# Kernel optimization log

Hardware: AMD Instinct MI355X
Metric: run time of the kernel (lower is better)

The kernel has to match this reference:

```python
import jax, jax.numpy as jnp
import numpy as np

N_HEAD = 16
N_KV_HEAD = 4


def setup_inputs() -> dict:
    key = jax.random.key(0)
    ks = jax.random.split(key, 5)
    B, T, D = 2, 2048, 2048
    kdim = D // N_HEAD  # 128
    s = 0.02
    x = jax.random.normal(ks[0], (B, T, D), dtype=jnp.float32)
    Wq = jax.random.normal(ks[1], (D, D), dtype=jnp.float32) * s
    Wk = jax.random.normal(ks[2], (D, N_KV_HEAD * kdim), dtype=jnp.float32) * s
    Wv = jax.random.normal(ks[3], (D, N_KV_HEAD * kdim), dtype=jnp.float32) * s
    Wo = jax.random.normal(ks[4], (D, D), dtype=jnp.float32) * s
    return {"x": x, "Wq": Wq, "Wk": Wk, "Wv": Wv, "Wo": Wo}


def reference(x, Wq, Wk, Wv, Wo):
    B, T, D = x.shape
    h, kv = N_HEAD, N_KV_HEAD
    g = h // kv  # query groups per kv head
    kdim = D // h
    Q = (x @ Wq).reshape(B, T, h, kdim).transpose(0, 2, 1, 3)   # [B,h,T,k]
    K = (x @ Wk).reshape(B, T, kv, kdim).transpose(0, 2, 1, 3)  # [B,kv,T,k]
    V = (x @ Wv).reshape(B, T, kv, kdim).transpose(0, 2, 1, 3)
    # repeat_interleave(g, dim=1): kv outer, group inner
    K = jnp.broadcast_to(K[:, :, None], (B, kv, g, T, kdim)).reshape(B, h, T, kdim)
    V = jnp.broadcast_to(V[:, :, None], (B, kv, g, T, kdim)).reshape(B, h, T, kdim)
    scores = jnp.einsum('bhqd,bhkd->bhqk', Q, K) / jnp.sqrt(jnp.float32(kdim))
    causal = jnp.tril(jnp.ones((T, T), dtype=bool))
    scores = jnp.where(causal[None, None], scores, jnp.float32(-jnp.inf))
    A = jax.nn.softmax(scores, axis=-1)
    Y = jnp.einsum('bhqk,bhkd->bhqd', A, V).transpose(0, 2, 1, 3).reshape(B, T, D)
    return Y @ Wo
```

## Files before the change

### kernel.cpp

```cpp
#include <hip/hip_runtime.h>
#include <hip/hip_bf16.h>

typedef __bf16 bf16x8 __attribute__((ext_vector_type(8)));
typedef float f32x4 __attribute__((ext_vector_type(4)));

__device__ __forceinline__ unsigned short f2bf(float f) {
  unsigned int u = __float_as_uint(f);
  u += 0x7fffu + ((u >> 16) & 1u);
  return (unsigned short)(u >> 16);
}

__device__ __forceinline__ unsigned int pack2(float lo, float hi) {
  __hip_bfloat162 h = __float22bfloat162_rn(float2{lo, hi});
  return *(unsigned int*)&h;
}

__device__ __forceinline__ void load_lds16(const void* g, void* l) {
  __builtin_amdgcn_global_load_lds(
      (const __attribute__((address_space(1))) unsigned int*)g,
      (__attribute__((address_space(3))) unsigned int*)l, 16, 0, 0);
}

__global__ void cvt_x(const float* __restrict__ in, unsigned short* __restrict__ out) {
  size_t i = ((size_t)blockIdx.x * 256 + threadIdx.x) * 4;
  float4 v = *(const float4*)(in + i);
  ushort4 o;
  o.x = f2bf(v.x); o.y = f2bf(v.y); o.z = f2bf(v.z); o.w = f2bf(v.w);
  *(ushort4*)(out + i) = o;
}

__global__ void tr_w(const float* __restrict__ in, unsigned short* __restrict__ out,
                     int ldin, int ldout) {
  __shared__ float tile[32][33];
  const int c0 = blockIdx.x * 32, r0 = blockIdx.y * 32;
  const int tx = threadIdx.x, ty = threadIdx.y;
#pragma unroll
  for (int j = 0; j < 4; ++j)
    tile[ty + j * 8][tx] = in[(size_t)(r0 + ty + j * 8) * ldin + c0 + tx];
  __syncthreads();
#pragma unroll
  for (int j = 0; j < 4; ++j)
    out[(size_t)(c0 + ty + j * 8) * ldout + r0 + tx] = f2bf(tile[tx][ty + j * 8]);
}

__global__ void tr_v(const unsigned short* __restrict__ QKV, unsigned short* __restrict__ VT) {
  __shared__ unsigned short tile[32][33];
  const int z = blockIdx.z, b = z >> 2, kvh = z & 3;
  const unsigned short* in = QKV + (size_t)(b * 2048) * 3072 + 2560 + kvh * 128;
  unsigned short* out = VT + (size_t)z * 128 * 2048;
  const int c0 = blockIdx.x * 32, r0 = blockIdx.y * 32;
  const int tx = threadIdx.x, ty = threadIdx.y;
#pragma unroll
  for (int j = 0; j < 4; ++j)
    tile[ty + j * 8][tx] = in[(size_t)(r0 + ty + j * 8) * 3072 + c0 + tx];
  __syncthreads();
#pragma unroll
  for (int j = 0; j < 4; ++j)
    out[(size_t)(c0 + ty + j * 8) * 2048 + r0 + tx] = tile[tx][ty + j * 8];
}

template <int NF, int OUTF32>
__global__ __launch_bounds__(512, 2) void gemm256(const unsigned short* __restrict__ A,
                                                  const unsigned short* __restrict__ B,
                                                  void* __restrict__ Cv, int M, int N, int K) {
  __shared__ __attribute__((aligned(16))) unsigned short Ah[2][2][256 * 32];
  __shared__ __attribute__((aligned(16))) unsigned short Bf[2][64 * NF * 64];
  const int tid = threadIdx.x;
  const int lane = tid & 63;
  const int cl = lane & 15, rg = lane >> 4;
  const int wave = tid >> 6;
  const int wm = wave >> 2, wn = wave & 3;
  const int bm = blockIdx.y, bn = blockIdx.x;
  const int NK = K >> 6;
  const int rowA = bm * 256, rowB = bn * (64 * NF);

  f32x4 acc[8][NF] = {};

  auto stage_A = [&](int bf, int h, int kt) {
#pragma unroll
    for (int i = 0; i < 2; ++i) {
      const int L = i * 512 + tid;
      const int r = L >> 2;
      const int c = (L & 3) ^ ((r >> 1) & 3);
      load_lds16(A + (size_t)(rowA + r) * K + kt * 64 + h * 32 + c * 8,
                 &Ah[bf][h][(size_t)(i * 512 + (tid & ~63)) * 8]);
    }
  };
  auto stage_B = [&](int bf, int kt) {
#pragma unroll
    for (int i = 0; i < NF; ++i) {
      const int L = i * 512 + tid;
      const int r = L >> 3;
      const int c = (L & 7) ^ (r & 7);
      load_lds16(B + (size_t)(rowB + r) * K + kt * 64 + c * 8,
                 &Bf[bf][(size_t)(i * 512 + (tid & ~63)) * 8]);
    }
  };

  stage_B(0, 0);
  stage_A(0, 0, 0);
  stage_A(0, 1, 0);
  __syncthreads();

  int buf = 0;
#pragma unroll 1
  for (int kt = 0; kt < NK; ++kt) {
    const bool nl = (kt + 1 < NK);
    if (nl) {
      stage_B(buf ^ 1, kt + 1);
      stage_A(buf ^ 1, 0, kt + 1);
      stage_A(buf ^ 1, 1, kt + 1);
    }
    {
      bf16x8 af[8], bfr[NF];
#pragma unroll
      for (int f = 0; f < 8; ++f) {
        const int r = 128 * wm + 16 * f + cl;
        af[f] = *(const bf16x8*)(&Ah[buf][0][(r * 4 + (rg ^ ((r >> 1) & 3))) * 8]);
      }
#pragma unroll
      for (int nf = 0; nf < NF; ++nf) {
        const int r = 16 * NF * wn + 16 * nf + cl;
        bfr[nf] = *(const bf16x8*)(&Bf[buf][(r * 8 + (rg ^ (r & 7))) * 8]);
      }
      __builtin_amdgcn_s_setprio(1);
#pragma unroll
      for (int f = 0; f < 8; ++f)
#pragma unroll
        for (int nf = 0; nf < NF; ++nf)
          acc[f][nf] = __builtin_amdgcn_mfma_f32_16x16x32_bf16(af[f], bfr[nf], acc[f][nf], 0, 0, 0);
      __builtin_amdgcn_s_setprio(0);
    }
    {
      bf16x8 af[8], bfr[NF];
#pragma unroll
      for (int f = 0; f < 8; ++f) {
        const int r = 128 * wm + 16 * f + cl;
        af[f] = *(const bf16x8*)(&Ah[buf][1][(r * 4 + (rg ^ ((r >> 1) & 3))) * 8]);
      }
#pragma unroll
      for (int nf = 0; nf < NF; ++nf) {
        const int r = 16 * NF * wn + 16 * nf + cl;
        bfr[nf] = *(const bf16x8*)(&Bf[buf][(r * 8 + ((4 + rg) ^ (r & 7))) * 8]);
      }
      __builtin_amdgcn_s_setprio(1);
#pragma unroll
      for (int f = 0; f < 8; ++f)
#pragma unroll
        for (int nf = 0; nf < NF; ++nf)
          acc[f][nf] = __builtin_amdgcn_mfma_f32_16x16x32_bf16(af[f], bfr[nf], acc[f][nf], 0, 0, 0);
      __builtin_amdgcn_s_setprio(0);
    }
    __syncthreads();
    buf ^= 1;
  }

#pragma unroll
  for (int f = 0; f < 8; ++f)
#pragma unroll
    for (int nf = 0; nf < NF; ++nf)
#pragma unroll
      for (int i = 0; i < 4; ++i) {
        const int row = bm * 256 + wm * 128 + f * 16 + rg * 4 + i;
        const int col = bn * 64 * NF + wn * 16 * NF + nf * 16 + cl;
        if (OUTF32)
          ((float*)Cv)[(size_t)row * N + col] = acc[f][nf][i];
        else
          ((unsigned short*)Cv)[(size_t)row * N + col] = f2bf(acc[f][nf][i]);
      }
}

__global__ __launch_bounds__(256, 2) void attn(const unsigned short* __restrict__ QKV,
                                               const unsigned short* __restrict__ VT,
                                               unsigned short* __restrict__ O) {
  __shared__ __attribute__((aligned(16))) unsigned short Ks[2][64 * 128];
  __shared__ __attribute__((aligned(16))) unsigned short VTs[2][128 * 64];
  const int T = 2048, LD = 3072, D = 2048;
  const int jp = blockIdx.x, h = blockIdx.y, b = blockIdx.z;
  const int kvh = h >> 2;
  const int tid = threadIdx.x, lane = tid & 63, wave = tid >> 6;
  const int cl = lane & 15, rg = lane >> 4;
  const bool abit = (lane & 16) != 0, bbit = (lane & 32) != 0;
  const bool ab = abit != bbit;
  const unsigned short* Kbase = QKV + (size_t)b * T * LD + 2048 + kvh * 128;
  const unsigned short* Vbase = VT + (size_t)(b * 4 + kvh) * 128 * T;

  auto stage = [&](int sb, int k0) {
#pragma unroll
    for (int i = 0; i < 4; ++i) {
      const int Ls = i * 256 + tid;
      const int r = Ls >> 4, s = Ls & 15, c = s ^ (r & 7);
      load_lds16(Kbase + (size_t)(k0 + r) * LD + c * 8,
                 &Ks[sb][(i * 256 + (tid & 0xC0)) * 8]);
    }
#pragma unroll
    for (int i = 0; i < 4; ++i) {
      const int Ls = i * 256 + tid;
      const int r = Ls >> 3, s = Ls & 7, c = s ^ (r & 7);
      load_lds16(Vbase + (size_t)r * T + k0 + c * 8,
                 &VTs[sb][(i * 256 + (tid & 0xC0)) * 8]);
    }
  };

  const float scale = 0.08838834764831845f;

#pragma unroll 1
  for (int pass = 0; pass < 2; ++pass) {
    const int jt = pass ? (31 - jp) : jp;
    const int q0 = jt * 64;
    const int nkt = jt + 1;
    const int qrow = q0 + wave * 16 + cl;

    const unsigned short* Qp = QKV + (size_t)(b * T + qrow) * LD + h * 128;
    bf16x8 qf[4];
#pragma unroll
    for (int ks = 0; ks < 4; ++ks) qf[ks] = *(const bf16x8*)(Qp + ks * 32 + rg * 8);

    f32x4 o[8] = {};
    float m = -1e30f, l = 0.f;
    int buf = 0;

    stage(0, 0);
    __syncthreads();

#pragma unroll 1
    for (int kt = 0; kt < nkt; ++kt) {
      if (kt + 1 < nkt) stage(buf ^ 1, (kt + 1) * 64);

      f32x4 sa[4] = {};
      __builtin_amdgcn_s_setprio(1);
#pragma unroll
      for (int ks = 0; ks < 4; ++ks) {
#pragma unroll
        for (int n = 0; n < 4; ++n) {
          const int row = n * 16 + cl;
          const int p = (ks * 4 + rg) ^ (row & 7);
          const bf16x8 kf = *(const bf16x8*)(&Ks[buf][row * 128 + p * 8]);
          sa[n] = __builtin_amdgcn_mfma_f32_16x16x32_bf16(kf, qf[ks], sa[n], 0, 0, 0);
        }
      }
      __builtin_amdgcn_s_setprio(0);

      const int k0 = kt * 64;
      float p[4][4];
      float pmax = -1e30f;
      if (kt == jt) {
#pragma unroll
        for (int n = 0; n < 4; ++n)
#pragma unroll
          for (int i = 0; i < 4; ++i) {
            const int kg = k0 + n * 16 + rg * 4 + i;
            p[n][i] = (kg > qrow) ? -1e30f : sa[n][i] * scale;
            pmax = fmaxf(pmax, p[n][i]);
          }
      } else {
#pragma unroll
        for (int n = 0; n < 4; ++n)
#pragma unroll
          for (int i = 0; i < 4; ++i) {
            p[n][i] = sa[n][i] * scale;
            pmax = fmaxf(pmax, p[n][i]);
          }
      }
      pmax = fmaxf(pmax, __shfl_xor(pmax, 16));
      pmax = fmaxf(pmax, __shfl_xor(pmax, 32));

      if (!__all(pmax <= m + 8.f)) {
        const float mnew = fmaxf(m, pmax);
        const float alpha = __expf(m - mnew);
        m = mnew;
        l *= alpha;
#pragma unroll
        for (int n2 = 0; n2 < 8; ++n2) o[n2] *= alpha;
      }

      float rs = 0.f;
#pragma unroll
      for (int n = 0; n < 4; ++n)
#pragma unroll
        for (int i = 0; i < 4; ++i) {
          p[n][i] = __expf(p[n][i] - m);
          rs += p[n][i];
        }
      rs += __shfl_xor(rs, 16);
      rs += __shfl_xor(rs, 32);
      l += rs;

      unsigned int F[2][4];
#pragma unroll
      for (int ks2 = 0; ks2 < 2; ++ks2) {
        const unsigned int pk00 = pack2(p[2 * ks2][0], p[2 * ks2][1]);
        const unsigned int pk01 = pack2(p[2 * ks2][2], p[2 * ks2][3]);
        const unsigned int pk10 = pack2(p[2 * ks2 + 1][0], p[2 * ks2 + 1][1]);
        const unsigned int pk11 = pack2(p[2 * ks2 + 1][2], p[2 * ks2 + 1][3]);
        const unsigned int s0 = bbit ? pk00 : pk10;
        const unsigned int s1 = bbit ? pk01 : pk11;
        const unsigned int r0 = (unsigned int)__shfl_xor((int)s0, 32);
        const unsigned int r1 = (unsigned int)__shfl_xor((int)s1, 32);
        const unsigned int gk0 = bbit ? pk10 : pk00;
        const unsigned int gk1 = bbit ? pk11 : pk01;
        const unsigned int t0 = ab ? gk0 : r0;
        const unsigned int t1 = ab ? gk1 : r1;
        const unsigned int u0 = (unsigned int)__shfl_xor((int)t0, 16);
        const unsigned int u1 = (unsigned int)__shfl_xor((int)t1, 16);
        const unsigned int k20 = ab ? r0 : gk0;
        const unsigned int k21 = ab ? r1 : gk1;
        F[ks2][0] = abit ? u0 : k20;
        F[ks2][1] = abit ? u1 : k21;
        F[ks2][2] = abit ? k20 : u0;
        F[ks2][3] = abit ? k21 : u1;
      }

      __builtin_amdgcn_s_setprio(1);
#pragma unroll
      for (int ks2 = 0; ks2 < 2; ++ks2) {
        uint4 fu = make_uint4(F[ks2][0], F[ks2][1], F[ks2][2], F[ks2][3]);
        const bf16x8 pf = *(const bf16x8*)&fu;
#pragma unroll
        for (int n2 = 0; n2 < 8; ++n2) {
          const int dr = n2 * 16 + cl;
          const int p2 = (ks2 * 4 + rg) ^ (dr & 7);
          const bf16x8 vf = *(const bf16x8*)(&VTs[buf][dr * 64 + p2 * 8]);
          o[n2] = __builtin_amdgcn_mfma_f32_16x16x32_bf16(vf, pf, o[n2], 0, 0, 0);
        }
      }
      __builtin_amdgcn_s_setprio(0);

      __syncthreads();
      buf ^= 1;
    }

    const float rl = __builtin_amdgcn_rcpf(l);
#pragma unroll
    for (int n2 = 0; n2 < 8; ++n2) {
      ushort4 ov;
      ov.x = f2bf(o[n2][0] * rl);
      ov.y = f2bf(o[n2][1] * rl);
      ov.z = f2bf(o[n2][2] * rl);
      ov.w = f2bf(o[n2][3] * rl);
      *(ushort4*)(O + (size_t)(b * T + qrow) * D + h * 128 + n2 * 16 + rg * 4) = ov;
    }
  }
}

extern "C" void kernel_launch(void* const* d_in, const int* in_sizes, int n_in,
                              void* d_out, int out_size, void* d_ws, size_t ws_size,
                              hipStream_t stream) {
  const float* x = (const float*)d_in[0];
  const float* Wq = (const float*)d_in[1];
  const float* Wk = (const float*)d_in[2];
  const float* Wv = (const float*)d_in[3];
  const float* Wo = (const float*)d_in[4];
  float* out = (float*)d_out;

  char* ws = (char*)d_ws;
  unsigned short* xb    = (unsigned short*)(ws);
  unsigned short* WqkvT = (unsigned short*)(ws + 16777216);
  unsigned short* WoT   = (unsigned short*)(ws + 29360128);
  unsigned short* QKV   = (unsigned short*)(ws + 37748736);
  unsigned short* VTb   = (unsigned short*)(ws + 62914560);

  cvt_x<<<dim3(8192), dim3(256), 0, stream>>>(x, xb);
  tr_w<<<dim3(64, 64), dim3(32, 8), 0, stream>>>(Wq, WqkvT, 2048, 2048);
  tr_w<<<dim3(16, 64), dim3(32, 8), 0, stream>>>(Wk, WqkvT + (size_t)2048 * 2048, 512, 2048);
  tr_w<<<dim3(16, 64), dim3(32, 8), 0, stream>>>(Wv, WqkvT + (size_t)2560 * 2048, 512, 2048);
  tr_w<<<dim3(64, 64), dim3(32, 8), 0, stream>>>(Wo, WoT, 2048, 2048);

  gemm256<3, 0><<<dim3(16, 16), dim3(512), 0, stream>>>(xb, WqkvT, QKV, 4096, 3072, 2048);
  tr_v<<<dim3(4, 64, 8), dim3(32, 8), 0, stream>>>(QKV, VTb);
  attn<<<dim3(16, 16, 2), dim3(256), 0, stream>>>(QKV, VTb, xb);
  gemm256<2, 1><<<dim3(16, 16), dim3(512), 0, stream>>>(xb, WoT, out, 4096, 2048, 2048);
}
```

Measured before the change: 200.4 us.

## Add 256x256-tile 8-phase ping-pong GEMM for the QKV projection

Adds a new GEMM kernel with 256x256 output tiles whose K loop is split into eight phases. Each phase interleaves LDS fragment reads and global-to-LDS prefetches with MFMA quarter-blocks, using explicit barriers and waitcnt fences. The QKV projection now uses it with a 12x16 grid instead of the 192-wide tile kernel on a 16x16 grid, raising arithmetic intensity per block and overlapping memory with compute. In exchange there are fewer blocks (192) on a GPU with many CUs, the manual waitcnt scheduling is fragile, and register pressure rises. Alongside this, unsigned short is renamed to a short alias.

```diff
diff --git a/kernel.cpp b/kernel.cpp
--- a/kernel.cpp
+++ b/kernel.cpp
@@ -3,11 +3,12 @@
 
 typedef __bf16 bf16x8 __attribute__((ext_vector_type(8)));
 typedef float f32x4 __attribute__((ext_vector_type(4)));
-
-__device__ __forceinline__ unsigned short f2bf(float f) {
+typedef unsigned short us;
+
+__device__ __forceinline__ us f2bf(float f) {
   unsigned int u = __float_as_uint(f);
   u += 0x7fffu + ((u >> 16) & 1u);
-  return (unsigned short)(u >> 16);
+  return (us)(u >> 16);
 }
 
 __device__ __forceinline__ unsigned int pack2(float lo, float hi) {
@@ -21,7 +22,7 @@
       (__attribute__((address_space(3))) unsigned int*)l, 16, 0, 0);
 }
 
-__global__ void cvt_x(const float* __restrict__ in, unsigned short* __restrict__ out) {
+__global__ void cvt_x(const float* __restrict__ in, us* __restrict__ out) {
   size_t i = ((size_t)blockIdx.x * 256 + threadIdx.x) * 4;
   float4 v = *(const float4*)(in + i);
   ushort4 o;
@@ -29,7 +30,7 @@
   *(ushort4*)(out + i) = o;
 }
 
-__global__ void tr_w(const float* __restrict__ in, unsigned short* __restrict__ out,
+__global__ void tr_w(const float* __restrict__ in, us* __restrict__ out,
                      int ldin, int ldout) {
   __shared__ float tile[32][33];
   const int c0 = blockIdx.x * 32, r0 = blockIdx.y * 32;
@@ -43,11 +44,11 @@
     out[(size_t)(c0 + ty + j * 8) * ldout + r0 + tx] = f2bf(tile[tx][ty + j * 8]);
 }
 
-__global__ void tr_v(const unsigned short* __restrict__ QKV, unsigned short* __restrict__ VT) {
-  __shared__ unsigned short tile[32][33];
+__global__ void tr_v(const us* __restrict__ QKV, us* __restrict__ VT) {
+  __shared__ us tile[32][33];
   const int z = blockIdx.z, b = z >> 2, kvh = z & 3;
-  const unsigned short* in = QKV + (size_t)(b * 2048) * 3072 + 2560 + kvh * 128;
-  unsigned short* out = VT + (size_t)z * 128 * 2048;
+  const us* in = QKV + (size_t)(b * 2048) * 3072 + 2560 + kvh * 128;
+  us* out = VT + (size_t)z * 128 * 2048;
   const int c0 = blockIdx.x * 32, r0 = blockIdx.y * 32;
   const int tx = threadIdx.x, ty = threadIdx.y;
 #pragma unroll
@@ -59,12 +60,153 @@
     out[(size_t)(c0 + ty + j * 8) * 2048 + r0 + tx] = tile[tx][ty + j * 8];
 }
 
+template <int OUTF32>
+__global__ __launch_bounds__(512, 2) void gemm8p(const us* __restrict__ A,
+                                                 const us* __restrict__ B,
+                                                 void* __restrict__ Cv,
+                                                 int M, int N, int K) {
+  __shared__ __attribute__((aligned(16))) us As[2][2][128 * 64];
+  __shared__ __attribute__((aligned(16))) us Bs[2][2][128 * 64];
+  const int tid = threadIdx.x;
+  const int lane = tid & 63;
+  const int cl = lane & 15, rg = lane >> 4;
+  const int wave = tid >> 6;
+  const int wm = wave >> 2, wn = wave & 3;
+  const int bm = blockIdx.y, bn = blockIdx.x;
+  const int NK = K >> 6;
+  const int rowA = bm * 256, rowB = bn * 256;
+
+  f32x4 acc[8][4] = {};
+
+  auto stA = [&](int bf, int h, int kt) {
+#pragma unroll
+    for (int i = 0; i < 2; ++i) {
+      const int L = i * 512 + tid;
+      const int r = L >> 3, c = (L & 7) ^ (r & 7);
+      load_lds16(A + (size_t)(rowA + h * 128 + r) * K + kt * 64 + c * 8,
+                 &As[bf][h][(i * 512 + (tid & ~63)) * 8]);
+    }
+  };
+  auto stB = [&](int bf, int h, int kt) {
+#pragma unroll
+    for (int i = 0; i < 2; ++i) {
+      const int L = i * 512 + tid;
+      const int r = L >> 3, c = (L & 7) ^ (r & 7);
+      load_lds16(B + (size_t)(rowB + h * 128 + r) * K + kt * 64 + c * 8,
+                 &Bs[bf][h][(i * 512 + (tid & ~63)) * 8]);
+    }
+  };
+
+  const int pxor = cl & 7;
+  bf16x8 aA[4][2], bA[2][2], bB[2][2];
+
+  auto rdA = [&](int bf, int fq) {
+#pragma unroll
+    for (int f = 0; f < 4; ++f) {
+      const int r = fq * 64 + f * 16 + cl;
+#pragma unroll
+      for (int ks = 0; ks < 2; ++ks)
+        aA[f][ks] = *(const bf16x8*)(&As[bf][wm][(r * 8 + ((ks * 4 + rg) ^ pxor)) * 8]);
+    }
+  };
+  auto rdB = [&](bf16x8 (&b)[2][2], int bf, int nq) {
+#pragma unroll
+    for (int j = 0; j < 2; ++j) {
+      const int r = (wn & 1) * 64 + (nq * 2 + j) * 16 + cl;
+#pragma unroll
+      for (int ks = 0; ks < 2; ++ks)
+        b[j][ks] = *(const bf16x8*)(&Bs[bf][wn >> 1][(r * 8 + ((ks * 4 + rg) ^ pxor)) * 8]);
+    }
+  };
+  auto mmQ = [&](bf16x8 (&b)[2][2], int fq, int nq) {
+    __builtin_amdgcn_s_setprio(1);
+#pragma unroll
+    for (int f = 0; f < 4; ++f)
+#pragma unroll
+      for (int j = 0; j < 2; ++j)
+#pragma unroll
+        for (int ks = 0; ks < 2; ++ks)
+          acc[fq * 4 + f][nq * 2 + j] = __builtin_amdgcn_mfma_f32_16x16x32_bf16(
+              aA[f][ks], b[j][ks], acc[fq * 4 + f][nq * 2 + j], 0, 0, 0);
+    __builtin_amdgcn_s_setprio(0);
+  };
+
+#define BAR __builtin_amdgcn_s_barrier()
+#define LGK0 asm volatile("s_waitcnt lgkmcnt(0)" ::: "memory")
+#define VM4 asm volatile("s_waitcnt vmcnt(4)" ::: "memory")
+#define VM0 asm volatile("s_waitcnt vmcnt(0)" ::: "memory")
+
+  stA(0, 0, 0); stB(0, 0, 0); stA(0, 1, 0); stB(0, 1, 0);
+  stB(1, 0, 1); stA(1, 0, 1);
+  VM4;
+  BAR;
+
+#pragma unroll 1
+  for (int T = 0; T < NK; T += 2) {
+    const bool s34 = (T + 2) < NK, s78 = (T + 3) < NK;
+
+    rdA(0, 0); rdB(bA, 0, 0);
+    stA(1, 1, T + 1);
+    asm volatile("s_waitcnt lgkmcnt(8)" ::: "memory");
+    BAR; LGK0; mmQ(bA, 0, 0); BAR;
+
+    rdB(bB, 0, 1);
+    stB(1, 1, T + 1);
+    BAR; LGK0; mmQ(bB, 0, 1); BAR;
+
+    rdA(0, 1);
+    if (s34) stB(0, 0, T + 2);
+    BAR; LGK0; mmQ(bA, 1, 0); BAR;
+
+    if (s34) stA(0, 0, T + 2);
+    BAR; mmQ(bB, 1, 1);
+    if (s34) { VM4; } else { VM0; }
+    BAR;
+
+    rdA(1, 0); rdB(bA, 1, 0);
+    if (s34) stB(0, 1, T + 2);
+    asm volatile("s_waitcnt lgkmcnt(8)" ::: "memory");
+    BAR; LGK0; mmQ(bA, 0, 0); BAR;
+
+    rdB(bB, 1, 1);
+    if (s34) stA(0, 1, T + 2);
+    BAR; LGK0; mmQ(bB, 0, 1); BAR;
+
+    rdA(1, 1);
+    if (s78) stB(1, 0, T + 3);
+    BAR; LGK0; mmQ(bA, 1, 0); BAR;
+
+    if (s78) stA(1, 0, T + 3);
+    BAR; mmQ(bB, 1, 1);
+    if (s78) { VM4; } else { VM0; }
+    BAR;
+  }
+#undef BAR
+#undef LGK0
+#undef VM4
+#undef VM0
+
+#pragma unroll
+  for (int f = 0; f < 8; ++f)
+#pragma unroll
+    for (int nf = 0; nf < 4; ++nf)
+#pragma unroll
+      for (int i = 0; i < 4; ++i) {
+        const int row = bm * 256 + wm * 128 + f * 16 + rg * 4 + i;
+        const int col = bn * 256 + wn * 64 + nf * 16 + cl;
+        if (OUTF32)
+          ((float*)Cv)[(size_t)row * N + col] = acc[f][nf][i];
+        else
+          ((us*)Cv)[(size_t)row * N + col] = f2bf(acc[f][nf][i]);
+      }
+}
+
 template <int NF, int OUTF32>
-__global__ __launch_bounds__(512, 2) void gemm256(const unsigned short* __restrict__ A,
-                                                  const unsigned short* __restrict__ B,
+__global__ __launch_bounds__(512, 2) void gemm256(const us* __restrict__ A,
+                                                  const us* __restrict__ B,
                                                   void* __restrict__ Cv, int M, int N, int K) {
-  __shared__ __attribute__((aligned(16))) unsigned short Ah[2][2][256 * 32];
-  __shared__ __attribute__((aligned(16))) unsigned short Bf[2][64 * NF * 64];
+  __shared__ __attribute__((aligned(16))) us Ah[2][2][256 * 32];
+  __shared__ __attribute__((aligned(16))) us Bf[2][64 * NF * 64];
   const int tid = threadIdx.x;
   const int lane = tid & 63;
   const int cl = lane & 15, rg = lane >> 4;
@@ -166,15 +308,15 @@
         if (OUTF32)
           ((float*)Cv)[(size_t)row * N + col] = acc[f][nf][i];
         else
-          ((unsigned short*)Cv)[(size_t)row * N + col] = f2bf(acc[f][nf][i]);
-      }
-}
-
-__global__ __launch_bounds__(256, 2) void attn(const unsigned short* __restrict__ QKV,
-                                               const unsigned short* __restrict__ VT,
-                                               unsigned short* __restrict__ O) {
-  __shared__ __attribute__((aligned(16))) unsigned short Ks[2][64 * 128];
-  __shared__ __attribute__((aligned(16))) unsigned short VTs[2][128 * 64];
+          ((us*)Cv)[(size_t)row * N + col] = f2bf(acc[f][nf][i]);
+      }
+}
+
+__global__ __launch_bounds__(256, 2) void attn(const us* __restrict__ QKV,
+                                               const us* __restrict__ VT,
+                                               us* __restrict__ O) {
+  __shared__ __attribute__((aligned(16))) us Ks[2][64 * 128];
+  __shared__ __attribute__((aligned(16))) us VTs[2][128 * 64];
   const int T = 2048, LD = 3072, D = 2048;
   const int jp = blockIdx.x, h = blockIdx.y, b = blockIdx.z;
   const int kvh = h >> 2;
@@ -182,8 +324,8 @@
   const int cl = lane & 15, rg = lane >> 4;
   const bool abit = (lane & 16) != 0, bbit = (lane & 32) != 0;
   const bool ab = abit != bbit;
-  const unsigned short* Kbase = QKV + (size_t)b * T * LD + 2048 + kvh * 128;
-  const unsigned short* Vbase = VT + (size_t)(b * 4 + kvh) * 128 * T;
+  const us* Kbase = QKV + (size_t)b * T * LD + 2048 + kvh * 128;
+  const us* Vbase = VT + (size_t)(b * 4 + kvh) * 128 * T;
 
   auto stage = [&](int sb, int k0) {
 #pragma unroll
@@ -211,7 +353,7 @@
     const int nkt = jt + 1;
     const int qrow = q0 + wave * 16 + cl;
 
-    const unsigned short* Qp = QKV + (size_t)(b * T + qrow) * LD + h * 128;
+    const us* Qp = QKV + (size_t)(b * T + qrow) * LD + h * 128;
     bf16x8 qf[4];
 #pragma unroll
     for (int ks = 0; ks < 4; ++ks) qf[ks] = *(const bf16x8*)(Qp + ks * 32 + rg * 8);
@@ -354,11 +496,11 @@
   float* out = (float*)d_out;
 
   char* ws = (char*)d_ws;
-  unsigned short* xb    = (unsigned short*)(ws);
-  unsigned short* WqkvT = (unsigned short*)(ws + 16777216);
-  unsigned short* WoT   = (unsigned short*)(ws + 29360128);
-  unsigned short* QKV   = (unsigned short*)(ws + 37748736);
-  unsigned short* VTb   = (unsigned short*)(ws + 62914560);
+  us* xb    = (us*)(ws);
+  us* WqkvT = (us*)(ws + 16777216);
+  us* WoT   = (us*)(ws + 29360128);
+  us* QKV   = (us*)(ws + 37748736);
+  us* VTb   = (us*)(ws + 62914560);
 
   cvt_x<<<dim3(8192), dim3(256), 0, stream>>>(x, xb);
   tr_w<<<dim3(64, 64), dim3(32, 8), 0, stream>>>(Wq, WqkvT, 2048, 2048);
@@ -366,7 +508,7 @@
   tr_w<<<dim3(16, 64), dim3(32, 8), 0, stream>>>(Wv, WqkvT + (size_t)2560 * 2048, 512, 2048);
   tr_w<<<dim3(64, 64), dim3(32, 8), 0, stream>>>(Wo, WoT, 2048, 2048);
 
-  gemm256<3, 0><<<dim3(16, 16), dim3(512), 0, stream>>>(xb, WqkvT, QKV, 4096, 3072, 2048);
+  gemm8p<0><<<dim3(12, 16), dim3(512), 0, stream>>>(xb, WqkvT, QKV, 4096, 3072, 2048);
   tr_v<<<dim3(4, 64, 8), dim3(32, 8), 0, stream>>>(QKV, VTb);
   attn<<<dim3(16, 16, 2), dim3(256), 0, stream>>>(QKV, VTb, xb);
   gemm256<2, 1><<<dim3(16, 16), dim3(512), 0, stream>>>(xb, WoT, out, 4096, 2048, 2048);
```

Result: slower. 208.4 us (+4.0%).

## Split causal attention key range into two halves with 128-row query tiles and merge

Applied to the files above, without the earlier changes.

Each attention block now handles a 128-row query tile, with each wave processing two 16-row subtiles. Every K/V fragment read from LDS therefore feeds two MFMAs. The causal key range of each tile is split into two equal halves run by separate blocks, which balances work per block. The halves write unnormalized bf16 partial outputs plus running max/sum, and a new merge_o kernel rescales and combines them. This costs an extra kernel launch and extra global traffic for the partials, which are stored in the output buffer and the freed weight workspace.

```diff
diff --git a/kernel.cpp b/kernel.cpp
--- a/kernel.cpp
+++ b/kernel.cpp
@@ -3,11 +3,16 @@
 
 typedef __bf16 bf16x8 __attribute__((ext_vector_type(8)));
 typedef float f32x4 __attribute__((ext_vector_type(4)));
-
-__device__ __forceinline__ unsigned short f2bf(float f) {
+typedef unsigned short us;
+
+__device__ __forceinline__ us f2bf(float f) {
   unsigned int u = __float_as_uint(f);
   u += 0x7fffu + ((u >> 16) & 1u);
-  return (unsigned short)(u >> 16);
+  return (us)(u >> 16);
+}
+
+__device__ __forceinline__ float bf2f(us u) {
+  return __uint_as_float(((unsigned int)u) << 16);
 }
 
 __device__ __forceinline__ unsigned int pack2(float lo, float hi) {
@@ -21,7 +26,7 @@
       (__attribute__((address_space(3))) unsigned int*)l, 16, 0, 0);
 }
 
-__global__ void cvt_x(const float* __restrict__ in, unsigned short* __restrict__ out) {
+__global__ void cvt_x(const float* __restrict__ in, us* __restrict__ out) {
   size_t i = ((size_t)blockIdx.x * 256 + threadIdx.x) * 4;
   float4 v = *(const float4*)(in + i);
   ushort4 o;
@@ -29,7 +34,7 @@
   *(ushort4*)(out + i) = o;
 }
 
-__global__ void tr_w(const float* __restrict__ in, unsigned short* __restrict__ out,
+__global__ void tr_w(const float* __restrict__ in, us* __restrict__ out,
                      int ldin, int ldout) {
   __shared__ float tile[32][33];
   const int c0 = blockIdx.x * 32, r0 = blockIdx.y * 32;
@@ -43,11 +48,11 @@
     out[(size_t)(c0 + ty + j * 8) * ldout + r0 + tx] = f2bf(tile[tx][ty + j * 8]);
 }
 
-__global__ void tr_v(const unsigned short* __restrict__ QKV, unsigned short* __restrict__ VT) {
-  __shared__ unsigned short tile[32][33];
+__global__ void tr_v(const us* __restrict__ QKV, us* __restrict__ VT) {
+  __shared__ us tile[32][33];
   const int z = blockIdx.z, b = z >> 2, kvh = z & 3;
-  const unsigned short* in = QKV + (size_t)(b * 2048) * 3072 + 2560 + kvh * 128;
-  unsigned short* out = VT + (size_t)z * 128 * 2048;
+  const us* in = QKV + (size_t)(b * 2048) * 3072 + 2560 + kvh * 128;
+  us* out = VT + (size_t)z * 128 * 2048;
   const int c0 = blockIdx.x * 32, r0 = blockIdx.y * 32;
   const int tx = threadIdx.x, ty = threadIdx.y;
 #pragma unroll
@@ -60,11 +65,11 @@
 }
 
 template <int NF, int OUTF32>
-__global__ __launch_bounds__(512, 2) void gemm256(const unsigned short* __restrict__ A,
-                                                  const unsigned short* __restrict__ B,
+__global__ __launch_bounds__(512, 2) void gemm256(const us* __restrict__ A,
+                                                  const us* __restrict__ B,
                                                   void* __restrict__ Cv, int M, int N, int K) {
-  __shared__ __attribute__((aligned(16))) unsigned short Ah[2][2][256 * 32];
-  __shared__ __attribute__((aligned(16))) unsigned short Bf[2][64 * NF * 64];
+  __shared__ __attribute__((aligned(16))) us Ah[2][2][256 * 32];
+  __shared__ __attribute__((aligned(16))) us Bf[2][64 * NF * 64];
   const int tid = threadIdx.x;
   const int lane = tid & 63;
   const int cl = lane & 15, rg = lane >> 4;
@@ -166,26 +171,30 @@
         if (OUTF32)
           ((float*)Cv)[(size_t)row * N + col] = acc[f][nf][i];
         else
-          ((unsigned short*)Cv)[(size_t)row * N + col] = f2bf(acc[f][nf][i]);
-      }
-}
-
-__global__ __launch_bounds__(256, 2) void attn(const unsigned short* __restrict__ QKV,
-                                               const unsigned short* __restrict__ VT,
-                                               unsigned short* __restrict__ O) {
-  __shared__ __attribute__((aligned(16))) unsigned short Ks[2][64 * 128];
-  __shared__ __attribute__((aligned(16))) unsigned short VTs[2][128 * 64];
-  const int T = 2048, LD = 3072, D = 2048;
-  const int jp = blockIdx.x, h = blockIdx.y, b = blockIdx.z;
+          ((us*)Cv)[(size_t)row * N + col] = f2bf(acc[f][nf][i]);
+      }
+}
+
+__global__ __launch_bounds__(256, 2) void attn(const us* __restrict__ QKV,
+                                               const us* __restrict__ VT,
+                                               us* __restrict__ Opart,
+                                               float2* __restrict__ ML) {
+  __shared__ __attribute__((aligned(16))) us Ks[2][64 * 128];
+  __shared__ __attribute__((aligned(16))) us VTs[2][128 * 64];
+  const int T = 2048, LD = 3072;
+  const int jt = 15 - (blockIdx.x & 15);
+  const int half = blockIdx.x >> 4;
+  const int h = blockIdx.y, b = blockIdx.z;
   const int kvh = h >> 2;
   const int tid = threadIdx.x, lane = tid & 63, wave = tid >> 6;
   const int cl = lane & 15, rg = lane >> 4;
   const bool abit = (lane & 16) != 0, bbit = (lane & 32) != 0;
   const bool ab = abit != bbit;
-  const unsigned short* Kbase = QKV + (size_t)b * T * LD + 2048 + kvh * 128;
-  const unsigned short* Vbase = VT + (size_t)(b * 4 + kvh) * 128 * T;
-
-  auto stage = [&](int sb, int k0) {
+  const us* Kbase = QKV + (size_t)b * T * LD + 2048 + kvh * 128;
+  const us* Vbase = VT + (size_t)(b * 4 + kvh) * 128 * T;
+
+  auto stage = [&](int sb, int kt) {
+    const int k0 = kt * 64;
 #pragma unroll
     for (int i = 0; i < 4; ++i) {
       const int Ls = i * 256 + tid;
@@ -203,75 +212,82 @@
   };
 
   const float scale = 0.08838834764831845f;
+  const int q0 = jt * 128;
+  const int qb = q0 + wave * 32;
+  const int kb = half ? (jt + 1) : 0;
+  const int ke = half ? (2 * jt + 2) : (jt + 1);
+
+  bf16x8 qf[2][4];
+#pragma unroll
+  for (int sub = 0; sub < 2; ++sub) {
+    const us* Qp = QKV + (size_t)(b * T + qb + sub * 16 + cl) * LD + h * 128;
+#pragma unroll
+    for (int ks = 0; ks < 4; ++ks) qf[sub][ks] = *(const bf16x8*)(Qp + ks * 32 + rg * 8);
+  }
+
+  f32x4 o[2][8] = {};
+  float mrun[2] = {-1e30f, -1e30f}, lrun[2] = {0.f, 0.f};
+  int buf = 0;
+
+  stage(0, kb);
+  __syncthreads();
 
 #pragma unroll 1
-  for (int pass = 0; pass < 2; ++pass) {
-    const int jt = pass ? (31 - jp) : jp;
-    const int q0 = jt * 64;
-    const int nkt = jt + 1;
-    const int qrow = q0 + wave * 16 + cl;
-
-    const unsigned short* Qp = QKV + (size_t)(b * T + qrow) * LD + h * 128;
-    bf16x8 qf[4];
-#pragma unroll
-    for (int ks = 0; ks < 4; ++ks) qf[ks] = *(const bf16x8*)(Qp + ks * 32 + rg * 8);
-
-    f32x4 o[8] = {};
-    float m = -1e30f, l = 0.f;
-    int buf = 0;
-
-    stage(0, 0);
-    __syncthreads();
-
-#pragma unroll 1
-    for (int kt = 0; kt < nkt; ++kt) {
-      if (kt + 1 < nkt) stage(buf ^ 1, (kt + 1) * 64);
-
-      f32x4 sa[4] = {};
-      __builtin_amdgcn_s_setprio(1);
-#pragma unroll
-      for (int ks = 0; ks < 4; ++ks) {
-#pragma unroll
-        for (int n = 0; n < 4; ++n) {
-          const int row = n * 16 + cl;
-          const int p = (ks * 4 + rg) ^ (row & 7);
-          const bf16x8 kf = *(const bf16x8*)(&Ks[buf][row * 128 + p * 8]);
-          sa[n] = __builtin_amdgcn_mfma_f32_16x16x32_bf16(kf, qf[ks], sa[n], 0, 0, 0);
-        }
-      }
-      __builtin_amdgcn_s_setprio(0);
-
-      const int k0 = kt * 64;
-      float p[4][4];
+  for (int kt = kb; kt < ke; ++kt) {
+    if (kt + 1 < ke) stage(buf ^ 1, kt + 1);
+
+    f32x4 sa[2][4] = {};
+    __builtin_amdgcn_s_setprio(1);
+#pragma unroll
+    for (int ks = 0; ks < 4; ++ks) {
+#pragma unroll
+      for (int n = 0; n < 4; ++n) {
+        const int row = n * 16 + cl;
+        const int p = (ks * 4 + rg) ^ (row & 7);
+        const bf16x8 kf = *(const bf16x8*)(&Ks[buf][row * 128 + p * 8]);
+        sa[0][n] = __builtin_amdgcn_mfma_f32_16x16x32_bf16(kf, qf[0][ks], sa[0][n], 0, 0, 0);
+        sa[1][n] = __builtin_amdgcn_mfma_f32_16x16x32_bf16(kf, qf[1][ks], sa[1][n], 0, 0, 0);
+      }
+    }
+    __builtin_amdgcn_s_setprio(0);
+
+    const int k0 = kt * 64;
+    float p[2][4][4];
+    unsigned int F[2][2][4];
+
+#pragma unroll
+    for (int sub = 0; sub < 2; ++sub) {
+      const int qbs = qb + sub * 16;
+      const int qrow = qbs + cl;
       float pmax = -1e30f;
-      if (kt == jt) {
+      if (k0 + 63 > qbs) {
 #pragma unroll
         for (int n = 0; n < 4; ++n)
 #pragma unroll
           for (int i = 0; i < 4; ++i) {
             const int kg = k0 + n * 16 + rg * 4 + i;
-            p[n][i] = (kg > qrow) ? -1e30f : sa[n][i] * scale;
-            pmax = fmaxf(pmax, p[n][i]);
+            p[sub][n][i] = (kg > qrow) ? -1e30f : sa[sub][n][i] * scale;
+            pmax = fmaxf(pmax, p[sub][n][i]);
           }
       } else {
 #pragma unroll
         for (int n = 0; n < 4; ++n)
 #pragma unroll
           for (int i = 0; i < 4; ++i) {
-            p[n][i] = sa[n][i] * scale;
-            pmax = fmaxf(pmax, p[n][i]);
+            p[sub][n][i] = sa[sub][n][i] * scale;
+            pmax = fmaxf(pmax, p[sub][n][i]);
           }
       }
       pmax = fmaxf(pmax, __shfl_xor(pmax, 16));
       pmax = fmaxf(pmax, __shfl_xor(pmax, 32));
 
-      if (!__all(pmax <= m + 8.f)) {
-        const float mnew = fmaxf(m, pmax);
-        const float alpha = __expf(m - mnew);
-        m = mnew;
-        l *= alpha;
-#pragma unroll
-        for (int n2 = 0; n2 < 8; ++n2) o[n2] *= alpha;
+      if (!__all(pmax <= mrun[sub] + 8.f)) {
+        const float mnew = fmaxf(mrun[sub], pmax);
+        const float alpha = __expf(mrun[sub] - mnew);
+        mrun[sub] = mnew;
+        lrun[sub] *= alpha;
+#pragma unroll
+        for (int n2 = 0; n2 < 8; ++n2) o[sub][n2] *= alpha;
       }
 
       float rs = 0.f;
@@ -279,20 +295,19 @@
       for (int n = 0; n < 4; ++n)
 #pragma unroll
         for (int i = 0; i < 4; ++i) {
-          p[n][i] = __expf(p[n][i] - m);
-          rs += p[n][i];
+          p[sub][n][i] = __expf(p[sub][n][i] - mrun[sub]);
+          rs += p[sub][n][i];
         }
       rs += __shfl_xor(rs, 16);
       rs += __shfl_xor(rs, 32);
-      l += rs;
-
-      unsigned int F[2][4];
+      lrun[sub] += rs;
+
 #pragma unroll
       for (int ks2 = 0; ks2 < 2; ++ks2) {
-        const unsigned int pk00 = pack2(p[2 * ks2][0], p[2 * ks2][1]);
-        const unsigned int pk01 = pack2(p[2 * ks2][2], p[2 * ks2][3]);
-        const unsigned int pk10 = pack2(p[2 * ks2 + 1][0], p[2 * ks2 + 1][1]);
-        const unsigned int pk11 = pack2(p[2 * ks2 + 1][2], p[2 * ks2 + 1][3]);
+        const unsigned int pk00 = pack2(p[sub][2 * ks2][0], p[sub][2 * ks2][1]);
+        const unsigned int pk01 = pack2(p[sub][2 * ks2][2], p[sub][2 * ks2][3]);
+        const unsigned int pk10 = pack2(p[sub][2 * ks2 + 1][0], p[sub][2 * ks2 + 1][1]);
+        const unsigned int pk11 = pack2(p[sub][2 * ks2 + 1][2], p[sub][2 * ks2 + 1][3]);
         const unsigned int s0 = bbit ? pk00 : pk10;
         const unsigned int s1 = bbit ? pk01 : pk11;
         const unsigned int r0 = (unsigned int)__shfl_xor((int)s0, 32);
@@ -305,42 +320,88 @@
         const unsigned int u1 = (unsigned int)__shfl_xor((int)t1, 16);
         const unsigned int k20 = ab ? r0 : gk0;
         const unsigned int k21 = ab ? r1 : gk1;
-        F[ks2][0] = abit ? u0 : k20;
-        F[ks2][1] = abit ? u1 : k21;
-        F[ks2][2] = abit ? k20 : u0;
-        F[ks2][3] = abit ? k21 : u1;
-      }
-
-      __builtin_amdgcn_s_setprio(1);
-#pragma unroll
-      for (int ks2 = 0; ks2 < 2; ++ks2) {
-        uint4 fu = make_uint4(F[ks2][0], F[ks2][1], F[ks2][2], F[ks2][3]);
-        const bf16x8 pf = *(const bf16x8*)&fu;
-#pragma unroll
-        for (int n2 = 0; n2 < 8; ++n2) {
-          const int dr = n2 * 16 + cl;
-          const int p2 = (ks2 * 4 + rg) ^ (dr & 7);
-          const bf16x8 vf = *(const bf16x8*)(&VTs[buf][dr * 64 + p2 * 8]);
-          o[n2] = __builtin_amdgcn_mfma_f32_16x16x32_bf16(vf, pf, o[n2], 0, 0, 0);
-        }
-      }
-      __builtin_amdgcn_s_setprio(0);
-
-      __syncthreads();
-      buf ^= 1;
-    }
-
-    const float rl = __builtin_amdgcn_rcpf(l);
+        F[sub][ks2][0] = abit ? u0 : k20;
+        F[sub][ks2][1] = abit ? u1 : k21;
+        F[sub][ks2][2] = abit ? k20 : u0;
+        F[sub][ks2][3] = abit ? k21 : u1;
+      }
+    }
+
+    __builtin_amdgcn_s_setprio(1);
+#pragma unroll
+    for (int ks2 = 0; ks2 < 2; ++ks2) {
+      uint4 f0 = make_uint4(F[0][ks2][0], F[0][ks2][1], F[0][ks2][2], F[0][ks2][3]);
+      uint4 f1 = make_uint4(F[1][ks2][0], F[1][ks2][1], F[1][ks2][2], F[1][ks2][3]);
+      const bf16x8 pf0 = *(const bf16x8*)&f0;
+      const bf16x8 pf1 = *(const bf16x8*)&f1;
+#pragma unroll
+      for (int n2 = 0; n2 < 8; ++n2) {
+        const int dr = n2 * 16 + cl;
+        const int p2 = (ks2 * 4 + rg) ^ (dr & 7);
+        const bf16x8 vf = *(const bf16x8*)(&VTs[buf][dr * 64 + p2 * 8]);
+        o[0][n2] = __builtin_amdgcn_mfma_f32_16x16x32_bf16(vf, pf0, o[0][n2], 0, 0, 0);
+        o[1][n2] = __builtin_amdgcn_mfma_f32_16x16x32_bf16(vf, pf1, o[1][n2], 0, 0, 0);
+      }
+    }
+    __builtin_amdgcn_s_setprio(0);
+
+    __syncthreads();
+    buf ^= 1;
+  }
+
+  us* Op = Opart + (size_t)half * 8388608;
+#pragma unroll
+  for (int sub = 0; sub < 2; ++sub) {
+    const int qrow = qb + sub * 16 + cl;
 #pragma unroll
     for (int n2 = 0; n2 < 8; ++n2) {
       ushort4 ov;
-      ov.x = f2bf(o[n2][0] * rl);
-      ov.y = f2bf(o[n2][1] * rl);
-      ov.z = f2bf(o[n2][2] * rl);
-      ov.w = f2bf(o[n2][3] * rl);
-      *(ushort4*)(O + (size_t)(b * T + qrow) * D + h * 128 + n2 * 16 + rg * 4) = ov;
+      ov.x = f2bf(o[sub][n2][0]);
+      ov.y = f2bf(o[sub][n2][1]);
+      ov.z = f2bf(o[sub][n2][2]);
+      ov.w = f2bf(o[sub][n2][3]);
+      *(ushort4*)(Op + (size_t)(b * T + qrow) * 2048 + h * 128 + n2 * 16 + rg * 4) = ov;
     }
   }
+  if (lane < 16) {
+#pragma unroll
+    for (int sub = 0; sub < 2; ++sub) {
+      const int q = qb + sub * 16 + lane;
+      ML[half * 65536 + ((b * 16 + h) * 2048 + q)] = float2{mrun[sub], lrun[sub]};
+    }
+  }
+}
+
+__global__ void merge_o(const us* __restrict__ Op, const float2* __restrict__ ML,
+                        us* __restrict__ O) {
+  const int idx = blockIdx.x * 256 + threadIdx.x;
+  const int row = idx >> 8;
+  const int col = (idx & 255) * 8;
+  const int h = col >> 7;
+  const int b = row >> 11, q = row & 2047;
+  const int mlrow = (b * 16 + h) * 2048 + q;
+  const float2 ml0 = ML[mlrow];
+  const float2 ml1 = ML[65536 + mlrow];
+  const float m = fmaxf(ml0.x, ml1.x);
+  const float a0 = __expf(ml0.x - m), a1 = __expf(ml1.x - m);
+  const float rl = __builtin_amdgcn_rcpf(ml0.y * a0 + ml1.y * a1);
+  const float s0 = a0 * rl, s1 = a1 * rl;
+  const size_t base = (size_t)row * 2048 + col;
+  const ushort4 x0 = *(const ushort4*)(Op + base);
+  const ushort4 x1 = *(const ushort4*)(Op + base + 4);
+  const ushort4 y0 = *(const ushort4*)(Op + 8388608 + base);
+  const ushort4 y1 = *(const ushort4*)(Op + 8388608 + base + 4);
+  ushort4 o0, o1;
+  o0.x = f2bf(bf2f(x0.x) * s0 + bf2f(y0.x) * s1);
+  o0.y = f2bf(bf2f(x0.y) * s0 + bf2f(y0.y) * s1);
+  o0.z = f2bf(bf2f(x0.z) * s0 + bf2f(y0.z) * s1);
+  o0.w = f2bf(bf2f(x0.w) * s0 + bf2f(y0.w) * s1);
+  o1.x = f2bf(bf2f(x1.x) * s0 + bf2f(y1.x) * s1);
+  o1.y = f2bf(bf2f(x1.y) * s0 + bf2f(y1.y) * s1);
+  o1.z = f2bf(bf2f(x1.z) * s0 + bf2f(y1.z) * s1);
+  o1.w = f2bf(bf2f(x1.w) * s0 + bf2f(y1.w) * s1);
+  *(ushort4*)(O + base) = o0;
+  *(ushort4*)(O + base + 4) = o1;
 }
 
 extern "C" void kernel_launch(void* const* d_in, const int* in_sizes, int n_in,
@@ -354,11 +415,13 @@
   float* out = (float*)d_out;
 
   char* ws = (char*)d_ws;
-  unsigned short* xb    = (unsigned short*)(ws);
-  unsigned short* WqkvT = (unsigned short*)(ws + 16777216);
-  unsigned short* WoT   = (unsigned short*)(ws + 29360128);
-  unsigned short* QKV   = (unsigned short*)(ws + 37748736);
-  unsigned short* VTb   = (unsigned short*)(ws + 62914560);
+  us* xb    = (us*)(ws);
+  us* WqkvT = (us*)(ws + 16777216);
+  us* WoT   = (us*)(ws + 29360128);
+  us* QKV   = (us*)(ws + 37748736);
+  us* VTb   = (us*)(ws + 62914560);
+  float2* ML = (float2*)(ws + 16777216);
+  us* Opart  = (us*)d_out;
 
   cvt_x<<<dim3(8192), dim3(256), 0, stream>>>(x, xb);
   tr_w<<<dim3(64, 64), dim3(32, 8), 0, stream>>>(Wq, WqkvT, 2048, 2048);
@@ -368,6 +431,7 @@
 
   gemm256<3, 0><<<dim3(16, 16), dim3(512), 0, stream>>>(xb, WqkvT, QKV, 4096, 3072, 2048);
   tr_v<<<dim3(4, 64, 8), dim3(32, 8), 0, stream>>>(QKV, VTb);
-  attn<<<dim3(16, 16, 2), dim3(256), 0, stream>>>(QKV, VTb, xb);
+  attn<<<dim3(32, 16, 2), dim3(256), 0, stream>>>(QKV, VTb, Opart, ML);
+  merge_o<<<dim3(4096), dim3(256), 0, stream>>>(Opart, ML, xb);
   gemm256<2, 1><<<dim3(16, 16), dim3(512), 0, stream>>>(xb, WoT, out, 4096, 2048, 2048);
 }
```

After: 244.3 us. +21.9%, slower.

## Split GEMM K-step into half-phases with staggered prefetch and fine-grained vmcnt waits

Applied to the files above, without the earlier changes.

Restructures the gemm256 main loop so the next tile's B loads are issued after the first half's LDS reads and the A loads after the second half's reads. Explicit s_waitcnt vmcnt counts and raw s_barrier replace the single __syncthreads per iteration. The goal is to overlap global-to-LDS traffic with MFMA work and avoid draining all outstanding loads at each barrier. It relies on hand-counted vmcnt values matching the number of outstanding direct-to-LDS loads, which is fragile and adds more barriers per iteration.

```diff
diff --git a/kernel.cpp b/kernel.cpp
--- a/kernel.cpp
+++ b/kernel.cpp
@@ -3,11 +3,12 @@
 
 typedef __bf16 bf16x8 __attribute__((ext_vector_type(8)));
 typedef float f32x4 __attribute__((ext_vector_type(4)));
-
-__device__ __forceinline__ unsigned short f2bf(float f) {
+typedef unsigned short us;
+
+__device__ __forceinline__ us f2bf(float f) {
   unsigned int u = __float_as_uint(f);
   u += 0x7fffu + ((u >> 16) & 1u);
-  return (unsigned short)(u >> 16);
+  return (us)(u >> 16);
 }
 
 __device__ __forceinline__ unsigned int pack2(float lo, float hi) {
@@ -21,7 +22,7 @@
       (__attribute__((address_space(3))) unsigned int*)l, 16, 0, 0);
 }
 
-__global__ void cvt_x(const float* __restrict__ in, unsigned short* __restrict__ out) {
+__global__ void cvt_x(const float* __restrict__ in, us* __restrict__ out) {
   size_t i = ((size_t)blockIdx.x * 256 + threadIdx.x) * 4;
   float4 v = *(const float4*)(in + i);
   ushort4 o;
@@ -29,7 +30,7 @@
   *(ushort4*)(out + i) = o;
 }
 
-__global__ void tr_w(const float* __restrict__ in, unsigned short* __restrict__ out,
+__global__ void tr_w(const float* __restrict__ in, us* __restrict__ out,
                      int ldin, int ldout) {
   __shared__ float tile[32][33];
   const int c0 = blockIdx.x * 32, r0 = blockIdx.y * 32;
@@ -43,11 +44,11 @@
     out[(size_t)(c0 + ty + j * 8) * ldout + r0 + tx] = f2bf(tile[tx][ty + j * 8]);
 }
 
-__global__ void tr_v(const unsigned short* __restrict__ QKV, unsigned short* __restrict__ VT) {
-  __shared__ unsigned short tile[32][33];
+__global__ void tr_v(const us* __restrict__ QKV, us* __restrict__ VT) {
+  __shared__ us tile[32][33];
   const int z = blockIdx.z, b = z >> 2, kvh = z & 3;
-  const unsigned short* in = QKV + (size_t)(b * 2048) * 3072 + 2560 + kvh * 128;
-  unsigned short* out = VT + (size_t)z * 128 * 2048;
+  const us* in = QKV + (size_t)(b * 2048) * 3072 + 2560 + kvh * 128;
+  us* out = VT + (size_t)z * 128 * 2048;
   const int c0 = blockIdx.x * 32, r0 = blockIdx.y * 32;
   const int tx = threadIdx.x, ty = threadIdx.y;
 #pragma unroll
@@ -60,11 +61,11 @@
 }
 
 template <int NF, int OUTF32>
-__global__ __launch_bounds__(512, 2) void gemm256(const unsigned short* __restrict__ A,
-                                                  const unsigned short* __restrict__ B,
+__global__ __launch_bounds__(512, 2) void gemm256(const us* __restrict__ A,
+                                                  const us* __restrict__ B,
                                                   void* __restrict__ Cv, int M, int N, int K) {
-  __shared__ __attribute__((aligned(16))) unsigned short Ah[2][2][256 * 32];
-  __shared__ __attribute__((aligned(16))) unsigned short Bf[2][64 * NF * 64];
+  __shared__ __attribute__((aligned(16))) us Ah[2][2][256 * 32];
+  __shared__ __attribute__((aligned(16))) us Bf[2][64 * NF * 64];
   const int tid = threadIdx.x;
   const int lane = tid & 63;
   const int cl = lane & 15, rg = lane >> 4;
@@ -100,58 +101,66 @@
   stage_B(0, 0);
   stage_A(0, 0, 0);
   stage_A(0, 1, 0);
-  __syncthreads();
+  asm volatile("s_waitcnt vmcnt(2)" ::: "memory");
+  __builtin_amdgcn_s_barrier();
 
   int buf = 0;
 #pragma unroll 1
   for (int kt = 0; kt < NK; ++kt) {
     const bool nl = (kt + 1 < NK);
+    bf16x8 af[8], bfr[NF];
+
+#pragma unroll
+    for (int f = 0; f < 8; ++f) {
+      const int r = 128 * wm + 16 * f + cl;
+      af[f] = *(const bf16x8*)(&Ah[buf][0][(r * 4 + (rg ^ ((r >> 1) & 3))) * 8]);
+    }
+#pragma unroll
+    for (int nf = 0; nf < NF; ++nf) {
+      const int r = 16 * NF * wn + 16 * nf + cl;
+      bfr[nf] = *(const bf16x8*)(&Bf[buf][(r * 8 + (rg ^ (r & 7))) * 8]);
+    }
+    if (nl) stage_B(buf ^ 1, kt + 1);
+    __builtin_amdgcn_s_barrier();
+    asm volatile("s_waitcnt lgkmcnt(0)" ::: "memory");
+    __builtin_amdgcn_s_setprio(1);
+#pragma unroll
+    for (int f = 0; f < 8; ++f)
+#pragma unroll
+      for (int nf = 0; nf < NF; ++nf)
+        acc[f][nf] = __builtin_amdgcn_mfma_f32_16x16x32_bf16(af[f], bfr[nf], acc[f][nf], 0, 0, 0);
+    __builtin_amdgcn_s_setprio(0);
     if (nl) {
-      stage_B(buf ^ 1, kt + 1);
-      stage_A(buf ^ 1, 0, kt + 1);
-      stage_A(buf ^ 1, 1, kt + 1);
-    }
-    {
-      bf16x8 af[8], bfr[NF];
-#pragma unroll
-      for (int f = 0; f < 8; ++f) {
-        const int r = 128 * wm + 16 * f + cl;
-        af[f] = *(const bf16x8*)(&Ah[buf][0][(r * 4 + (rg ^ ((r >> 1) & 3))) * 8]);
-      }
-#pragma unroll
-      for (int nf = 0; nf < NF; ++nf) {
-        const int r = 16 * NF * wn + 16 * nf + cl;
-        bfr[nf] = *(const bf16x8*)(&Bf[buf][(r * 8 + (rg ^ (r & 7))) * 8]);
-      }
-      __builtin_amdgcn_s_setprio(1);
-#pragma unroll
-      for (int f = 0; f < 8; ++f)
-#pragma unroll
-        for (int nf = 0; nf < NF; ++nf)
-          acc[f][nf] = __builtin_amdgcn_mfma_f32_16x16x32_bf16(af[f], bfr[nf], acc[f][nf], 0, 0, 0);
-      __builtin_amdgcn_s_setprio(0);
-    }
-    {
-      bf16x8 af[8], bfr[NF];
-#pragma unroll
-      for (int f = 0; f < 8; ++f) {
-        const int r = 128 * wm + 16 * f + cl;
-        af[f] = *(const bf16x8*)(&Ah[buf][1][(r * 4 + (rg ^ ((r >> 1) & 3))) * 8]);
-      }
-#pragma unroll
-      for (int nf = 0; nf < NF; ++nf) {
-        const int r = 16 * NF * wn + 16 * nf + cl;
-        bfr[nf] = *(const bf16x8*)(&Bf[buf][(r * 8 + ((4 + rg) ^ (r & 7))) * 8]);
-      }
-      __builtin_amdgcn_s_setprio(1);
-#pragma unroll
-      for (int f = 0; f < 8; ++f)
-#pragma unroll
-        for (int nf = 0; nf < NF; ++nf)
-          acc[f][nf] = __builtin_amdgcn_mfma_f32_16x16x32_bf16(af[f], bfr[nf], acc[f][nf], 0, 0, 0);
-      __builtin_amdgcn_s_setprio(0);
-    }
-    __syncthreads();
+      if constexpr (NF == 3) { asm volatile("s_waitcnt vmcnt(3)" ::: "memory"); }
+      else                   { asm volatile("s_waitcnt vmcnt(2)" ::: "memory"); }
+    } else {
+      asm volatile("s_waitcnt vmcnt(0)" ::: "memory");
+    }
+    __builtin_amdgcn_s_barrier();
+
+#pragma unroll
+    for (int f = 0; f < 8; ++f) {
+      const int r = 128 * wm + 16 * f + cl;
+      af[f] = *(const bf16x8*)(&Ah[buf][1][(r * 4 + (rg ^ ((r >> 1) & 3))) * 8]);
+    }
+#pragma unroll
+    for (int nf = 0; nf < NF; ++nf) {
+      const int r = 16 * NF * wn + 16 * nf + cl;
+      bfr[nf] = *(const bf16x8*)(&Bf[buf][(r * 8 + ((4 + rg) ^ (r & 7))) * 8]);
+    }
+    if (nl) { stage_A(buf ^ 1, 0, kt + 1); stage_A(buf ^ 1, 1, kt + 1); }
+    __builtin_amdgcn_s_barrier();
+    asm volatile("s_waitcnt lgkmcnt(0)" ::: "memory");
+    __builtin_amdgcn_s_setprio(1);
+#pragma unroll
+    for (int f = 0; f < 8; ++f)
+#pragma unroll
+      for (int nf = 0; nf < NF; ++nf)
+        acc[f][nf] = __builtin_amdgcn_mfma_f32_16x16x32_bf16(af[f], bfr[nf], acc[f][nf], 0, 0, 0);
+    __builtin_amdgcn_s_setprio(0);
+    if (nl) asm volatile("s_waitcnt vmcnt(2)" ::: "memory");
+    __builtin_amdgcn_s_barrier();
+
     buf ^= 1;
   }
 
@@ -166,15 +175,15 @@
         if (OUTF32)
           ((float*)Cv)[(size_t)row * N + col] = acc[f][nf][i];
         else
-          ((unsigned short*)Cv)[(size_t)row * N + col] = f2bf(acc[f][nf][i]);
-      }
-}
-
-__global__ __launch_bounds__(256, 2) void attn(const unsigned short* __restrict__ QKV,
-                                               const unsigned short* __restrict__ VT,
-                                               unsigned short* __restrict__ O) {
-  __shared__ __attribute__((aligned(16))) unsigned short Ks[2][64 * 128];
-  __shared__ __attribute__((aligned(16))) unsigned short VTs[2][128 * 64];
+          ((us*)Cv)[(size_t)row * N + col] = f2bf(acc[f][nf][i]);
+      }
+}
+
+__global__ __launch_bounds__(256, 2) void attn(const us* __restrict__ QKV,
+                                               const us* __restrict__ VT,
+                                               us* __restrict__ O) {
+  __shared__ __attribute__((aligned(16))) us Ks[2][64 * 128];
+  __shared__ __attribute__((aligned(16))) us VTs[2][128 * 64];
   const int T = 2048, LD = 3072, D = 2048;
   const int jp = blockIdx.x, h = blockIdx.y, b = blockIdx.z;
   const int kvh = h >> 2;
@@ -182,8 +191,8 @@
   const int cl = lane & 15, rg = lane >> 4;
   const bool abit = (lane & 16) != 0, bbit = (lane & 32) != 0;
   const bool ab = abit != bbit;
-  const unsigned short* Kbase = QKV + (size_t)b * T * LD + 2048 + kvh * 128;
-  const unsigned short* Vbase = VT + (size_t)(b * 4 + kvh) * 128 * T;
+  const us* Kbase = QKV + (size_t)b * T * LD + 2048 + kvh * 128;
+  const us* Vbase = VT + (size_t)(b * 4 + kvh) * 128 * T;
 
   auto stage = [&](int sb, int k0) {
 #pragma unroll
@@ -211,7 +220,7 @@
     const int nkt = jt + 1;
     const int qrow = q0 + wave * 16 + cl;
 
-    const unsigned short* Qp = QKV + (size_t)(b * T + qrow) * LD + h * 128;
+    const us* Qp = QKV + (size_t)(b * T + qrow) * LD + h * 128;
     bf16x8 qf[4];
 #pragma unroll
     for (int ks = 0; ks < 4; ++ks) qf[ks] = *(const bf16x8*)(Qp + ks * 32 + rg * 8);
@@ -354,11 +363,11 @@
   float* out = (float*)d_out;
 
   char* ws = (char*)d_ws;
-  unsigned short* xb    = (unsigned short*)(ws);
-  unsigned short* WqkvT = (unsigned short*)(ws + 16777216);
-  unsigned short* WoT   = (unsigned short*)(ws + 29360128);
-  unsigned short* QKV   = (unsigned short*)(ws + 37748736);
-  unsigned short* VTb   = (unsigned short*)(ws + 62914560);
+  us* xb    = (us*)(ws);
+  us* WqkvT = (us*)(ws + 16777216);
+  us* WoT   = (us*)(ws + 29360128);
+  us* QKV   = (us*)(ws + 37748736);
+  us* VTb   = (us*)(ws + 62914560);
 
   cvt_x<<<dim3(8192), dim3(256), 0, stream>>>(x, xb);
   tr_w<<<dim3(64, 64), dim3(32, 8), 0, stream>>>(Wq, WqkvT, 2048, 2048);
```

Result: faster. 190.9 us (-4.7%).
